# Kernel tuning notes

Hardware: AMD Instinct MI355X
Metric: run time of the kernel (lower is better)

## Reference

```python
import jax, jax.numpy as jnp
import numpy as np

PI = 3.141592653589793


def conv2d(x, w, b=None, padding=0, groups=1):
    out = jax.lax.conv_general_dilated(
        x, w, window_strides=(1, 1), padding=((padding, padding), (padding, padding)),
        dimension_numbers=('NCHW', 'OIHW', 'NCHW'), feature_group_count=groups)
    if b is not None:
        out = out + b.reshape(1, -1, 1, 1)
    return out


def group_norm(x, weight, bias, num_groups, eps=1e-5):
    B, C, H, W = x.shape
    xg = x.reshape(B, num_groups, C // num_groups, H, W)
    mean = xg.mean(axis=(2, 3, 4), keepdims=True)
    var = xg.var(axis=(2, 3, 4), keepdims=True)
    xg = (xg - mean) / jnp.sqrt(var + eps)
    return xg.reshape(B, C, H, W) * weight.reshape(1, -1, 1, 1) + bias.reshape(1, -1, 1, 1)


def l2norm(x, eps=1e-12):
    n = jnp.sqrt(jnp.sum(x * x, axis=1, keepdims=True))
    return x / jnp.maximum(n, eps)


def dense_sift(x):
    # kornia DenseSIFTDescriptor defaults: 8 angle bins, 4x4 spatial bins, bin size 4,
    # stride 1, padding 1, rootsift=True, clipval=0.2. Input (B,1,H,W) -> (B,128,H,W).
    eps = 1e-10
    B, C, H, W = x.shape
    # spatial_gradient(x, 'diff'), normalized: central differences / 2, replicate pad
    p = jnp.pad(x, ((0, 0), (0, 0), (1, 1), (1, 1)), mode='edge')
    gx = (p[:, :, 1:-1, 2:] - p[:, :, 1:-1, :-2]) * 0.5
    gy = (p[:, :, 2:, 1:-1] - p[:, :, :-2, 1:-1]) * 0.5
    mag = jnp.sqrt(gx * gx + gy * gy + eps)
    ori = jnp.arctan2(gy, gx + eps) + 2.0 * PI
    o_big = 8.0 * ori / (2.0 * PI)
    bo0f = jnp.floor(o_big)
    wo1 = o_big - bo0f
    bo0 = bo0f % 8
    bo1 = (bo0 + 1) % 8
    wo0m = (1.0 - wo1) * mag
    wo1m = wo1 * mag
    bins = jnp.arange(8, dtype=x.dtype).reshape(1, 8, 1, 1)
    # soft orientation-histogram binning -> (B,8,H,W)
    ang = jnp.where(bo0 == bins, wo0m, 0.0) + jnp.where(bo1 == bins, wo1m, 0.0)
    # triangular bin pooling kernel (ksize=4), depthwise conv, pad 2 -> (B,8,H+1,W+1)
    ks2 = 2.0
    xc2 = ks2 - jnp.abs(jnp.arange(4, dtype=x.dtype) + 0.5 - ks2)
    pk = jnp.outer(xc2, xc2) / (ks2 ** 2)
    pk = jnp.tile(pk.reshape(1, 1, 4, 4), (8, 1, 1, 1))
    pooled = jax.lax.conv_general_dilated(
        ang, pk, (1, 1), ((2, 2), (2, 2)),
        dimension_numbers=('NCHW', 'OIHW', 'NCHW'), feature_group_count=8)
    # PoolingConv with identity reshape kernel (k=4, pad=1) == 4x4 patch extraction
    pp = jnp.pad(pooled, ((0, 0), (0, 0), (1, 1), (1, 1)))
    patches = jnp.stack([pp[:, :, y:y + H, xx:xx + W]
                         for y in range(4) for xx in range(4)], axis=2)  # (B,8,16,H,W)
    out = patches.reshape(B, 128, H, W)
    out = jnp.clip(l2norm(out), 0.0, 0.2)
    out = l2norm(out)
    # rootsift: sqrt(L1-normalized + eps)
    l1 = jnp.sum(jnp.abs(out), axis=1, keepdims=True)
    out = jnp.sqrt(out / jnp.maximum(l1, 1e-12) + eps)
    return out


def gauss1d(ks, sigma):
    t = jnp.arange(ks, dtype=jnp.float32) - (ks - 1) / 2.0
    g = jnp.exp(-(t * t) / (2.0 * sigma * sigma))
    return g / g.sum()


def joint_bilateral_blur(inp, guidance, ks=5, sigma_color=0.1, sigma_space=(1.5, 1.5)):
    # kornia joint_bilateral_blur: border_type='reflect', color_distance_type='l1'
    B, C, H, W = inp.shape
    pad = ks // 2
    pi_ = jnp.pad(inp, ((0, 0), (0, 0), (pad, pad), (pad, pad)), mode='reflect')
    pg = jnp.pad(guidance, ((0, 0), (0, 0), (pad, pad), (pad, pad)), mode='reflect')

    def unfold(p):  # (B,C,H,W,ks*ks), flatten order (dy, dx)
        return jnp.stack([p[:, :, y:y + H, x:x + W]
                          for y in range(ks) for x in range(ks)], axis=-1)

    ui = unfold(pi_)
    ug = unfold(pg)
    diff = ug - guidance[..., None]
    cdist_sq = jnp.square(jnp.sum(jnp.abs(diff), axis=1, keepdims=True))  # L1 over channels, squared
    color_k = jnp.exp(-0.5 / (sigma_color ** 2) * cdist_sq)               # (B,1,H,W,K2)
    space_k = jnp.outer(gauss1d(ks, sigma_space[0]), gauss1d(ks, sigma_space[1])).reshape(1, 1, 1, 1, -1)
    kernel = space_k * color_k
    return (ui * kernel).sum(-1) / kernel.sum(-1)


def setup_inputs() -> dict:
    key = jax.random.key(0)
    ks = jax.random.split(key, 8)
    B, H, W = 4, 270, 512

    def wgt(k, shape, scale=0.05):
        return jax.random.normal(k, shape, dtype=jnp.float32) * scale

    z = lambda n: jnp.zeros((n,), dtype=jnp.float32)
    o = lambda n: jnp.ones((n,), dtype=jnp.float32)
    return {
        'x': jax.random.normal(ks[0], (B, 1, H, W), dtype=jnp.float32),
        'w1': wgt(ks[1], (64, 128, 5, 5)), 'b1': z(64), 'g1w': o(64), 'g1b': z(64),
        'w2': wgt(ks[2], (32, 64, 3, 3)), 'b2': z(32), 'g2w': o(32), 'g2b': z(32),
        'w3': wgt(ks[3], (16, 32, 3, 3)), 'b3': z(16), 'g3w': o(16), 'g3b': z(16),
        'w4': wgt(ks[4], (8, 16, 3, 3)), 'b4': z(8), 'g4w': o(8), 'g4b': z(8),
        'w5': wgt(ks[5], (2, 8, 3, 3)), 'b5': z(2),
        'sw1': wgt(ks[6], (32, 128, 1, 1)), 'sb1': z(32),
        'sw2': wgt(ks[7], (8, 32, 1, 1)), 'sb2': z(8),
    }


def reference(x, w1, b1, g1w, g1b, w2, b2, g2w, g2b, w3, b3, g3w, g3b,
              w4, b4, g4w, g4b, w5, b5, sw1, sb1, sw2, sb2):
    orig = x
    s = dense_sift(x)                                     # (B,128,H,W)
    h = jax.nn.relu(group_norm(conv2d(s, w1, b1, 2), g1w, g1b, 8))
    h = jax.nn.relu(group_norm(conv2d(h, w2, b2, 1), g2w, g2b, 8))
    h = h + conv2d(s, sw1, sb1, 0)                        # skip 1
    blk = h
    h = jax.nn.relu(group_norm(conv2d(h, w3, b3, 1), g3w, g3b, 4))
    h = jax.nn.relu(group_norm(conv2d(h, w4, b4, 1), g4w, g4b, 4))
    h = h + conv2d(blk, sw2, sb2, 0)                      # skip 2
    h = conv2d(h, w5, b5, 1)                              # (B,2,H,W)
    guide = jnp.tile(orig, (1, 2, 1, 1))
    h = joint_bilateral_blur(h, guide, ks=5, sigma_color=0.1, sigma_space=(1.5, 1.5))
    h = jnp.tanh(h)
    scale = jnp.array([0.436, 0.615], dtype=h.dtype).reshape(1, 2, 1, 1)
    return h * scale
```

## Files before the change

kernel.cpp:

```cpp
#include <hip/hip_runtime.h>

#define DEV __device__ __forceinline__

typedef __bf16 bf16x8 __attribute__((ext_vector_type(8)));
typedef float f32x4 __attribute__((ext_vector_type(4)));

union U8 { uint4 q; unsigned short u[8]; };

constexpr int BN = 4, H = 270, W = 512, HW = H * W;
constexpr int IH5 = 274, P5 = 516;
constexpr int IH3 = 272, P3 = 514;

DEV unsigned short f2bf(float f) {
  unsigned int u = __builtin_bit_cast(unsigned int, f);
  u = (u + 0x7FFFu + ((u >> 16) & 1u)) >> 16;
  return (unsigned short)u;
}
DEV float bf2f(unsigned short h) {
  return __builtin_bit_cast(float, (unsigned int)h << 16);
}

#define GLL16(g, l)                                                                        \
  __builtin_amdgcn_global_load_lds((const __attribute__((address_space(1))) void*)(g),     \
                                   (__attribute__((address_space(3))) void*)(l), 16, 0, 0)

DEV int swz(int row) { return ((row >> 1) & 3) << 4; }

__global__ void k_fill(float* __restrict__ out, int n, float v) {
  int i = blockIdx.x * 256 + threadIdx.x;
  if (i < n) out[i] = v;
}

template <int C, int PD>
__global__ void k_halo(unsigned short* __restrict__ buf, int IHt, int pitch, int nb_) {
  int vPerRow = pitch * C / 8;
  int topBot = 2 * PD * vPerRow;
  int sideV = PD * C / 8;
  int midRows = IHt - 2 * PD;
  int perS = topBot + midRows * 2 * sideV;
  int v = blockIdx.x * 256 + threadIdx.x;
  if (v >= nb_ * perS) return;
  int s = v / perS, r = v % perS;
  size_t base = (size_t)s * IHt * pitch * C;
  size_t off;
  if (r < topBot) {
    int half = r / (PD * vPerRow);
    int rr = r % (PD * vPerRow);
    off = ((size_t)(half ? (IHt - PD) : 0) * pitch * C) + (size_t)rr * 8;
  } else {
    int r2 = r - topBot;
    int row = r2 / (2 * sideV), c2 = r2 % (2 * sideV);
    int side = c2 / sideV, cc = c2 % sideV;
    off = ((size_t)(PD + row) * pitch + (side ? (pitch - PD) : 0)) * C + (size_t)cc * 8;
  }
  *(uint4*)(buf + base + off) = uint4{0, 0, 0, 0};
}

__global__ void k_sift_ang(const float* __restrict__ x, float* __restrict__ ang, int nTot) {
  int p = blockIdx.x * 256 + threadIdx.x;
  if (p >= nTot) return;
  int b = p / HW, r = p % HW, y = r / W, xx = r % W;
  const float* xb = x + (size_t)b * HW;
  float xm = xb[y * W + (xx > 0 ? xx - 1 : 0)];
  float xp = xb[y * W + (xx < W - 1 ? xx + 1 : W - 1)];
  float ym = xb[(y > 0 ? y - 1 : 0) * W + xx];
  float yp = xb[(y < H - 1 ? y + 1 : H - 1) * W + xx];
  float gx = (xp - xm) * 0.5f, gy = (yp - ym) * 0.5f;
  float mag = sqrtf(gx * gx + gy * gy + 1e-10f);
  float ori = atan2f(gy, gx + 1e-10f) + 6.2831855f;
  float o = (8.0f * ori) / 6.2831855f;
  float bo0f = floorf(o);
  float wo1 = o - bo0f;
  int b0 = ((int)bo0f) & 7;
  int b1 = (b0 + 1) & 7;
  float w0m = (1.0f - wo1) * mag, w1m = wo1 * mag;
  float v[8];
#pragma unroll
  for (int k = 0; k < 8; ++k)
    v[k] = (k == b0 ? w0m : 0.0f) + (k == b1 ? w1m : 0.0f);
  float4* o4 = (float4*)(ang + (size_t)p * 8);
  o4[0] = make_float4(v[0], v[1], v[2], v[3]);
  o4[1] = make_float4(v[4], v[5], v[6], v[7]);
}

__global__ void k_sift_pool(const float* __restrict__ ang, float* __restrict__ pooled, int nTot) {
  constexpr int PH = H + 1, PW = W + 1;
  int p = blockIdx.x * 256 + threadIdx.x;
  if (p >= nTot) return;
  int b = p / (PH * PW), r = p % (PH * PW), y = r / PW, xx = r % PW;
  float4 a0 = {0, 0, 0, 0}, a1 = {0, 0, 0, 0};
  const float xc2[4] = {0.5f, 1.5f, 1.5f, 0.5f};
#pragma unroll
  for (int ky = 0; ky < 4; ++ky) {
    int yy = y - 2 + ky;
    if (yy < 0 || yy >= H) continue;
#pragma unroll
    for (int kx = 0; kx < 4; ++kx) {
      int xs = xx - 2 + kx;
      if (xs < 0 || xs >= W) continue;
      float w = xc2[ky] * xc2[kx] * 0.25f;
      const float4* s4 = (const float4*)(ang + ((size_t)(b * H + yy) * W + xs) * 8);
      float4 v0 = s4[0], v1 = s4[1];
      a0.x += w * v0.x; a0.y += w * v0.y; a0.z += w * v0.z; a0.w += w * v0.w;
      a1.x += w * v1.x; a1.y += w * v1.y; a1.z += w * v1.z; a1.w += w * v1.w;
    }
  }
  float4* o4 = (float4*)(pooled + (size_t)p * 8);
  o4[0] = a0; o4[1] = a1;
}

__global__ void k_sift_desc(const float* __restrict__ pooled, unsigned short* __restrict__ spad) {
  constexpr int PH = H + 1, PW = W + 1;
  int tid = threadIdx.x;
  int wv = tid >> 6, lane = tid & 63;
  int p = blockIdx.x * 4 + wv;
  int b = p / HW, r = p % HW, yy = r / W, xx = r % W;
  int a = lane >> 3, jj = lane & 7;
  int j0 = jj * 2;
  int dy = j0 >> 2, dx = j0 & 3;
  int rr = yy + dy - 1;
  int c0 = xx + dx - 1, c1 = c0 + 1;
  bool rv = (rr >= 0 && rr <= H);
  int rc = min(max(rr, 0), H);
  const float* pb = pooled + ((size_t)(b * PH + rc) * PW) * 8 + a;
  float v0 = 0.0f, v1 = 0.0f;
  if (rv && c0 >= 0 && c0 <= W) v0 = pb[(size_t)c0 * 8];
  if (rv && c1 >= 0 && c1 <= W) v1 = pb[(size_t)c1 * 8];

  float n2 = v0 * v0 + v1 * v1;
#pragma unroll
  for (int m = 1; m < 64; m <<= 1) n2 += __shfl_xor(n2, m);
  float inv = 1.0f / fmaxf(sqrtf(n2), 1e-12f);
  v0 = fminf(v0 * inv, 0.2f);
  v1 = fminf(v1 * inv, 0.2f);
  float n2b = v0 * v0 + v1 * v1;
#pragma unroll
  for (int m = 1; m < 64; m <<= 1) n2b += __shfl_xor(n2b, m);
  inv = 1.0f / fmaxf(sqrtf(n2b), 1e-12f);
  v0 *= inv; v1 *= inv;
  float l1 = v0 + v1;
#pragma unroll
  for (int m = 1; m < 64; m <<= 1) l1 += __shfl_xor(l1, m);
  float il1 = 1.0f / fmaxf(l1, 1e-12f);
  v0 = sqrtf(v0 * il1 + 1e-10f);
  v1 = sqrtf(v1 * il1 + 1e-10f);
  unsigned int pk = (unsigned int)f2bf(v0) | ((unsigned int)f2bf(v1) << 16);
  *(unsigned int*)(spad + ((size_t)(b * IH5 + yy + 2) * P5 + xx + 2) * 128 + lane * 2) = pk;
}

template <int CIN, int COUT, int KS>
__global__ void k_prep(const float* __restrict__ w, unsigned short* __restrict__ wbuf) {
  int i = blockIdx.x * 256 + threadIdx.x;
  if (i >= KS * KS * COUT * CIN) return;
  int t = i / (COUT * CIN), r2 = i % (COUT * CIN), co = r2 / CIN, e = r2 % CIN;
  wbuf[i] = f2bf(w[(co * CIN + e) * (KS * KS) + t]);
}

template <int CIN, int COUT, int KS, int NG, int PADOFF, int MINB, bool FSKIP>
__launch_bounds__(512, MINB)
__global__ void k_convr(const unsigned short* __restrict__ in, int IHt, int ipitch,
                        const unsigned short* __restrict__ wtap,
                        const float* __restrict__ bias,
                        const unsigned short* __restrict__ wsk,
                        const float* __restrict__ skb,
                        unsigned short* __restrict__ outraw,
                        unsigned short* __restrict__ skraw,
                        float* __restrict__ part, int nbid) {
  constexpr int SLABPX = 512 + KS - 1;
  constexpr int KQ = CIN / 32;
  constexpr int NF = COUT / 16;
  constexpr int SLAB = SLABPX * 64;
  constexpr int SWQ = COUT * 64;
  constexpr int SWROW = KS * SWQ;
  constexpr int SSK = FSKIP ? 32 * 64 : 16;
  __shared__ __align__(16) unsigned char slabB[2][SLAB];
  __shared__ __align__(16) unsigned char wrowB[2][SWROW];
  __shared__ __align__(16) unsigned char wskB[2][SSK];
  __shared__ float red[8][16];

  int tid = threadIdx.x;
  int lane = tid & 63, wid = tid >> 6;
  int l15 = lane & 15, hi = lane >> 4;

  int bid = blockIdx.x;
  int q8 = nbid >> 3, r8 = nbid & 7;
  int xcd = bid & 7;
  int by = (xcd < r8 ? xcd * (q8 + 1) : r8 * (q8 + 1) + (xcd - r8) * q8) + (bid >> 3);
  int y = by % H, b = by / H;

  f32x4 acc[4][NF] = {};
  f32x4 ask[4][2] = {};

  auto stage = [&](int it, int pbuf) {
    int q = it / KS, ky = it % KS;
    const char* src = (const char*)(in + ((size_t)(b * IHt + y + ky + PADOFF) * ipitch + PADOFF) * CIN + q * 32);
    for (int d = tid * 16; d < SLAB; d += 8192) {
      int px = d >> 6, qb = d & 63;
      GLL16(src + px * (CIN * 2) + (qb ^ swz(px)), slabB[pbuf] + d);
    }
    const char* wsrc = (const char*)wtap + (size_t)(ky * KS) * (COUT * CIN * 2) + q * 64;
    for (int d = tid * 16; d < SWROW; d += 8192) {
      int kx = d / SWQ, rem = d % SWQ;
      int co = rem >> 6, qb = rem & 63;
      GLL16(wsrc + (size_t)kx * (COUT * CIN * 2) + co * (CIN * 2) + (qb ^ swz(co)), wrowB[pbuf] + d);
    }
  };
  auto stage_wsk = [&](int q, int pbuf) {
    const char* src = (const char*)wsk + q * 64;
    for (int d = tid * 16; d < 32 * 64; d += 8192) {
      int co = d >> 6, qb = d & 63;
      GLL16(src + co * (CIN * 2) + (qb ^ swz(co)), wskB[pbuf] + d);
    }
  };

  stage(0, 0);
  if constexpr (FSKIP) stage_wsk(0, 0);
  __syncthreads();

#pragma unroll 1
  for (int it = 0; it < KQ * KS; ++it) {
    int cur = it & 1;
    int q = it / KS, ky = it % KS;
    if (it + 1 < KQ * KS) {
      stage(it + 1, cur ^ 1);
      if (FSKIP && (it + 1) % KS == 0) stage_wsk((it + 1) / KS, ((it + 1) / KS) & 1);
    }
    const unsigned char* sl = slabB[cur];
    const unsigned char* wr = wrowB[cur];
    int koff = hi * 16;
#pragma unroll
    for (int kx = 0; kx < KS; ++kx) {
      bf16x8 af[4];
#pragma unroll
      for (int mi = 0; mi < 4; ++mi) {
        int px = wid * 64 + mi * 16 + l15 + kx;
        af[mi] = *(const bf16x8*)(sl + px * 64 + (koff ^ swz(px)));
      }
#pragma unroll
      for (int ni = 0; ni < NF; ++ni) {
        int co = ni * 16 + l15;
        bf16x8 bq = *(const bf16x8*)(wr + kx * SWQ + co * 64 + (koff ^ swz(co)));
#pragma unroll
        for (int mi = 0; mi < 4; ++mi)
          acc[mi][ni] = __builtin_amdgcn_mfma_f32_16x16x32_bf16(af[mi], bq, acc[mi][ni], 0, 0, 0);
      }
      if constexpr (FSKIP) {
        if (ky == KS / 2 && kx == KS / 2) {
#pragma unroll
          for (int ni = 0; ni < 2; ++ni) {
            int co = ni * 16 + l15;
            bf16x8 bq = *(const bf16x8*)(wskB[q & 1] + co * 64 + (koff ^ swz(co)));
#pragma unroll
            for (int mi = 0; mi < 4; ++mi)
              ask[mi][ni] = __builtin_amdgcn_mfma_f32_16x16x32_bf16(af[mi], bq, ask[mi][ni], 0, 0, 0);
          }
        }
      }
    }
    __syncthreads();
  }

#pragma unroll
  for (int ni = 0; ni < NF; ++ni) {
    float bv = bias[ni * 16 + l15];
#pragma unroll
    for (int mi = 0; mi < 4; ++mi)
#pragma unroll
      for (int rr = 0; rr < 4; ++rr)
        acc[mi][ni][rr] += bv;
  }
  unsigned short* op = outraw + ((size_t)(b * H + y) * W) * COUT;
#pragma unroll
  for (int mi = 0; mi < 4; ++mi)
#pragma unroll
    for (int rr = 0; rr < 4; ++rr) {
      int px = wid * 64 + mi * 16 + hi * 4 + rr;
#pragma unroll
      for (int ni = 0; ni < NF; ++ni)
        op[(size_t)px * COUT + ni * 16 + l15] = f2bf(acc[mi][ni][rr]);
    }
  if constexpr (FSKIP) {
    unsigned short* ops = skraw + ((size_t)(b * H + y) * W) * 32;
#pragma unroll
    for (int ni = 0; ni < 2; ++ni) {
      float bv = skb[ni * 16 + l15];
#pragma unroll
      for (int mi = 0; mi < 4; ++mi)
#pragma unroll
        for (int rr = 0; rr < 4; ++rr)
          ask[mi][ni][rr] += bv;
    }
#pragma unroll
    for (int mi = 0; mi < 4; ++mi)
#pragma unroll
      for (int rr = 0; rr < 4; ++rr) {
        int px = wid * 64 + mi * 16 + hi * 4 + rr;
#pragma unroll
        for (int ni = 0; ni < 2; ++ni)
          ops[(size_t)px * 32 + ni * 16 + l15] = f2bf(ask[mi][ni][rr]);
      }
  }
  if constexpr (NG > 0) {
    constexpr int GPC = COUT / NG;
#pragma unroll
    for (int ni = 0; ni < NF; ++ni) {
      float s = 0.0f, q2 = 0.0f;
#pragma unroll
      for (int mi = 0; mi < 4; ++mi)
#pragma unroll
        for (int rr = 0; rr < 4; ++rr) {
          float v = acc[mi][ni][rr];
          s += v; q2 += v * v;
        }
      s += __shfl_xor(s, 16); q2 += __shfl_xor(q2, 16);
      s += __shfl_xor(s, 32); q2 += __shfl_xor(q2, 32);
#pragma unroll
      for (int m = 1; m < GPC; m <<= 1) { s += __shfl_xor(s, m); q2 += __shfl_xor(q2, m); }
      if (hi == 0 && (l15 % GPC) == 0) {
        int g = ni * (16 / GPC) + l15 / GPC;
        red[wid][g] = s;
        red[wid][NG + g] = q2;
      }
    }
    __syncthreads();
    if (tid < 2 * NG) {
      float t = 0.0f;
#pragma unroll
      for (int wv2 = 0; wv2 < 8; ++wv2) t += red[wv2][tid];
      part[(size_t)by * (2 * NG) + tid] = t;
    }
  }
}

template <int COUT, int NG>
__global__ void k_gn_fin(const float* __restrict__ part, int NB,
                         const float* __restrict__ gw, const float* __restrict__ gb,
                         float* __restrict__ scale, float* __restrict__ shift, float invN) {
  constexpr int GPC = COUT / NG;
  int b = blockIdx.x / NG, g = blockIdx.x % NG;
  int lane = threadIdx.x;
  float s = 0.0f, q = 0.0f;
  for (int i = lane; i < NB; i += 64) {
    const float* pp = part + (size_t)(b * NB + i) * (2 * NG);
    s += pp[g]; q += pp[NG + g];
  }
#pragma unroll
  for (int m = 1; m < 64; m <<= 1) { s += __shfl_xor(s, m); q += __shfl_xor(q, m); }
  if (lane == 0) {
    float mean = s * invN;
    float var = q * invN - mean * mean;
    float rstd = rsqrtf(var + 1e-5f);
#pragma unroll
    for (int j = 0; j < GPC; ++j) {
      int c = g * GPC + j;
      float sc = gw[c] * rstd;
      scale[b * COUT + c] = sc;
      shift[b * COUT + c] = gb[c] - mean * sc;
    }
  }
}

template <int C, bool ADDSKIP>
__global__ void k_norm(const unsigned short* __restrict__ raw,
                       const unsigned short* __restrict__ skip,
                       const float* __restrict__ scale, const float* __restrict__ shift,
                       unsigned short* __restrict__ outpad) {
  int e = blockIdx.x * 256 + threadIdx.x;
  int idx = e * 8;
  int p = idx / C, c0 = idx % C;
  int b = p / HW, r = p % HW, y = r / W, xx = r % W;
  U8 v; v.q = *(const uint4*)(raw + (size_t)p * C + c0);
  U8 sk;
  if (ADDSKIP) sk.q = *(const uint4*)(skip + (size_t)p * C + c0);
  const float* sc = scale + b * C + c0;
  const float* sh = shift + b * C + c0;
  U8 o;
#pragma unroll
  for (int j = 0; j < 8; ++j) {
    float f = fmaxf(bf2f(v.u[j]) * sc[j] + sh[j], 0.0f);
    if (ADDSKIP) f += bf2f(sk.u[j]);
    o.u[j] = f2bf(f);
  }
  *(uint4*)(outpad + ((size_t)(b * IH3 + y + 1) * P3 + xx + 1) * C + c0) = o.q;
}

__global__ void k_conv4(const unsigned short* __restrict__ h3pad, const float* __restrict__ w4,
                        const float* __restrict__ b4, unsigned short* __restrict__ h4raw,
                        float* __restrict__ part) {
  __shared__ float wl[1152];
  __shared__ float red[4][8];
  for (int i = threadIdx.x; i < 1152; i += 256) {
    int t = i / 128, r2 = i % 128, ci = r2 >> 3, co = r2 & 7;
    wl[i] = w4[(co * 16 + ci) * 9 + t];
  }
  __syncthreads();
  int p = blockIdx.x * 256 + threadIdx.x;
  int b = p / HW, r = p % HW, y = r / W, xx = r % W;
  float acc[8];
#pragma unroll
  for (int co = 0; co < 8; ++co) acc[co] = b4[co];
#pragma unroll
  for (int t = 0; t < 9; ++t) {
    int ky = t / 3, kx = t % 3;
    const unsigned short* ip = h3pad + ((size_t)(b * IH3 + y + ky) * P3 + (xx + kx)) * 16;
    U8 u0, u1;
    u0.q = *(const uint4*)ip;
    u1.q = *(const uint4*)(ip + 8);
#pragma unroll
    for (int ci = 0; ci < 16; ++ci) {
      float iv = bf2f(ci < 8 ? u0.u[ci] : u1.u[ci - 8]);
#pragma unroll
      for (int co = 0; co < 8; ++co)
        acc[co] += iv * wl[t * 128 + ci * 8 + co];
    }
  }
  int lane = threadIdx.x & 63, wv = threadIdx.x >> 6;
  float s[4], q[4];
#pragma unroll
  for (int g = 0; g < 4; ++g) {
    s[g] = acc[2 * g] + acc[2 * g + 1];
    q[g] = acc[2 * g] * acc[2 * g] + acc[2 * g + 1] * acc[2 * g + 1];
  }
#pragma unroll
  for (int m = 1; m < 64; m <<= 1) {
#pragma unroll
    for (int g = 0; g < 4; ++g) { s[g] += __shfl_xor(s[g], m); q[g] += __shfl_xor(q[g], m); }
  }
  if (lane == 0) {
#pragma unroll
    for (int g = 0; g < 4; ++g) { red[wv][g] = s[g]; red[wv][4 + g] = q[g]; }
  }
  __syncthreads();
  if (threadIdx.x < 8)
    part[(size_t)blockIdx.x * 8 + threadIdx.x] =
        red[0][threadIdx.x] + red[1][threadIdx.x] + red[2][threadIdx.x] + red[3][threadIdx.x];
  U8 o;
#pragma unroll
  for (int co = 0; co < 8; ++co) o.u[co] = f2bf(acc[co]);
  *(uint4*)(h4raw + (size_t)p * 8) = o.q;
}

__global__ void k_norm4(const unsigned short* __restrict__ h4raw, const unsigned short* __restrict__ blkpad,
                        const float* __restrict__ scale, const float* __restrict__ shift,
                        const float* __restrict__ sw2, const float* __restrict__ sb2,
                        unsigned short* __restrict__ blk2pad) {
  __shared__ float wl[256];
  {
    int i = threadIdx.x;
    int ci = i >> 3, co = i & 7;
    wl[i] = sw2[co * 32 + ci];
  }
  __syncthreads();
  int p = blockIdx.x * 256 + threadIdx.x;
  int b = p / HW, r = p % HW, y = r / W, xx = r % W;
  float acc[8];
#pragma unroll
  for (int co = 0; co < 8; ++co) acc[co] = sb2[co];
  size_t cbase = ((size_t)(b * IH3 + y + 1) * P3 + (xx + 1));
  const unsigned short* bp = blkpad + cbase * 32;
#pragma unroll
  for (int half = 0; half < 4; ++half) {
    U8 u; u.q = *(const uint4*)(bp + half * 8);
#pragma unroll
    for (int j = 0; j < 8; ++j) {
      float iv = bf2f(u.u[j]);
      int ci = half * 8 + j;
#pragma unroll
      for (int co = 0; co < 8; ++co) acc[co] += iv * wl[ci * 8 + co];
    }
  }
  U8 hv; hv.q = *(const uint4*)(h4raw + (size_t)p * 8);
  U8 o;
#pragma unroll
  for (int co = 0; co < 8; ++co) {
    float f = fmaxf(bf2f(hv.u[co]) * scale[b * 8 + co] + shift[b * 8 + co], 0.0f) + acc[co];
    o.u[co] = f2bf(f);
  }
  *(uint4*)(blk2pad + cbase * 8) = o.q;
}

__global__ void k_conv5(const unsigned short* __restrict__ blk2pad, const float* __restrict__ w5,
                        const float* __restrict__ b5, float* __restrict__ h5) {
  __shared__ float wl[144];
  if (threadIdx.x < 144) {
    int i = threadIdx.x;
    int t = i / 16, r2 = i % 16, ci = r2 >> 1, co = r2 & 1;
    wl[i] = w5[(co * 8 + ci) * 9 + t];
  }
  __syncthreads();
  int p = blockIdx.x * 256 + threadIdx.x;
  int b = p / HW, r = p % HW, y = r / W, xx = r % W;
  float a0 = b5[0], a1 = b5[1];
#pragma unroll
  for (int t = 0; t < 9; ++t) {
    int ky = t / 3, kx = t % 3;
    const unsigned short* ip = blk2pad + ((size_t)(b * IH3 + y + ky) * P3 + (xx + kx)) * 8;
    U8 u; u.q = *(const uint4*)ip;
#pragma unroll
    for (int ci = 0; ci < 8; ++ci) {
      float iv = bf2f(u.u[ci]);
      a0 += iv * wl[t * 16 + ci * 2];
      a1 += iv * wl[t * 16 + ci * 2 + 1];
    }
  }
  h5[(size_t)p * 2] = a0;
  h5[(size_t)p * 2 + 1] = a1;
}

__global__ void k_bilateral(const float* __restrict__ h5, const float* __restrict__ x,
                            float* __restrict__ out, int nTot) {
  int p = blockIdx.x * 256 + threadIdx.x;
  if (p >= nTot) return;
  int b = p / HW, r = p % HW, y = r / W, xx = r % W;
  const float* xb = x + (size_t)b * HW;
  float xc = xb[r];
  float e1 = expf(-1.0f / 4.5f), e0 = expf(-4.0f / 4.5f);
  float gs = 1.0f + 2.0f * e1 + 2.0f * e0;
  float g[5] = {e0 / gs, e1 / gs, 1.0f / gs, e1 / gs, e0 / gs};
  float n0 = 0.0f, n1 = 0.0f, den = 0.0f;
#pragma unroll
  for (int dy = 0; dy < 5; ++dy) {
    int yn = y + dy - 2;
    yn = yn < 0 ? -yn : (yn >= H ? 2 * H - 2 - yn : yn);
#pragma unroll
    for (int dx = 0; dx < 5; ++dx) {
      int xn = xx + dx - 2;
      xn = xn < 0 ? -xn : (xn >= W ? 2 * W - 2 - xn : xn);
      float xv = xb[yn * W + xn];
      float d = xv - xc;
      float wgt = g[dy] * g[dx] * expf(-200.0f * d * d);
      den += wgt;
      const float* hp = h5 + ((size_t)(b * HW) + yn * W + xn) * 2;
      n0 += wgt * hp[0];
      n1 += wgt * hp[1];
    }
  }
  float o0 = tanhf(n0 / den) * 0.436f;
  float o1 = tanhf(n1 / den) * 0.615f;
  out[(size_t)(b * 2) * HW + r] = o0;
  out[(size_t)(b * 2 + 1) * HW + r] = o1;
}

extern "C" void kernel_launch(void* const* d_in, const int* in_sizes, int n_in,
                              void* d_out, int out_size, void* d_ws, size_t ws_size,
                              hipStream_t stream) {
  (void)in_sizes; (void)n_in; (void)out_size;
  const float* x   = (const float*)d_in[0];
  const float* w1  = (const float*)d_in[1];
  const float* b1  = (const float*)d_in[2];
  const float* g1w = (const float*)d_in[3];
  const float* g1b = (const float*)d_in[4];
  const float* w2  = (const float*)d_in[5];
  const float* b2  = (const float*)d_in[6];
  const float* g2w = (const float*)d_in[7];
  const float* g2b = (const float*)d_in[8];
  const float* w3  = (const float*)d_in[9];
  const float* b3  = (const float*)d_in[10];
  const float* g3w = (const float*)d_in[11];
  const float* g3b = (const float*)d_in[12];
  const float* w4  = (const float*)d_in[13];
  const float* b4  = (const float*)d_in[14];
  const float* g4w = (const float*)d_in[15];
  const float* g4b = (const float*)d_in[16];
  const float* w5  = (const float*)d_in[17];
  const float* b5  = (const float*)d_in[18];
  const float* sw1 = (const float*)d_in[19];
  const float* sb1 = (const float*)d_in[20];
  const float* sw2 = (const float*)d_in[21];
  const float* sb2 = (const float*)d_in[22];
  float* out = (float*)d_out;
  char* ws = (char*)d_ws;

  auto AL = [](size_t v) { return (v + 255) & ~(size_t)255; };
  const size_t sSPAD  = (size_t)IH5 * P5 * 128 * 2;
  const size_t sANG   = (size_t)HW * 8 * 4;
  const size_t sH1RAW = (size_t)HW * 64 * 2;
  const size_t sH1PAD = (size_t)IH3 * P3 * 64 * 2;
  const size_t sH2RAW = (size_t)HW * 32 * 2;
  const size_t sBLKP  = (size_t)IH3 * P3 * 32 * 2;
  const size_t sH3RAW = (size_t)HW * 16 * 2;
  const size_t sH3PAD = (size_t)IH3 * P3 * 16 * 2;
  const size_t sH4RAW = (size_t)HW * 8 * 2;
  const size_t sBLK2  = (size_t)IH3 * P3 * 8 * 2;

  int nb = 0;
  size_t offB = 0, offH1PAD = 0, offSmall = 0;
  const size_t smallFixed = AL(1024 * 1024) + AL((size_t)4 * 1080 * 16 * 4) + 8 * 4096;
  for (int cand = 4; cand >= 1; cand >>= 1) {
    size_t oB   = AL((size_t)cand * sSPAD);
    size_t oH1P = AL(oB + (size_t)cand * sH1RAW);
    size_t oS   = AL(oH1P + (size_t)cand * sH1PAD);
    size_t need = oS + smallFixed + AL((size_t)cand * sH2RAW);
    if (ws_size >= need) { nb = cand; offB = oB; offH1PAD = oH1P; offSmall = oS; break; }
  }
  if (nb == 0) {
    k_fill<<<(BN * 2 * HW + 255) / 256, 256, 0, stream>>>(out, BN * 2 * HW, 123.0f);
    return;
  }

  size_t oWB1  = offSmall;
  size_t oWB2  = AL(oWB1 + 25 * 64 * 128 * 2);
  size_t oWB3  = AL(oWB2 + 9 * 32 * 64 * 2);
  size_t oWBS  = AL(oWB3 + 9 * 16 * 32 * 2);
  size_t oPART = AL(oWBS + 32 * 128 * 2);
  size_t oSC1  = AL(oPART + (size_t)4 * 1080 * 16 * 4);
  size_t oSC2  = oSC1 + 4096, oSC3 = oSC2 + 4096, oSC4 = oSC3 + 4096;
  size_t oSK1  = oSC4 + 4096;

  unsigned short* wb1  = (unsigned short*)(ws + oWB1);
  unsigned short* wb2  = (unsigned short*)(ws + oWB2);
  unsigned short* wb3  = (unsigned short*)(ws + oWB3);
  unsigned short* wbs1 = (unsigned short*)(ws + oWBS);
  float* part = (float*)(ws + oPART);
  float* sc1 = (float*)(ws + oSC1); float* sh1 = sc1 + nb * 64;
  float* sc2 = (float*)(ws + oSC2); float* sh2 = sc2 + nb * 32;
  float* sc3 = (float*)(ws + oSC3); float* sh3 = sc3 + nb * 16;
  float* sc4 = (float*)(ws + oSC4); float* sh4 = sc4 + nb * 8;
  unsigned short* sk1 = (unsigned short*)(ws + oSK1);

  k_prep<128, 64, 5><<<800, 256, 0, stream>>>(w1, wb1);
  k_prep<64, 32, 3><<<72, 256, 0, stream>>>(w2, wb2);
  k_prep<32, 16, 3><<<18, 256, 0, stream>>>(w3, wb3);
  k_prep<128, 32, 1><<<16, 256, 0, stream>>>(sw1, wbs1);

  size_t t0 = AL((size_t)nb * sBLKP);
  size_t t1 = AL(t0 + (size_t)nb * sH3RAW);
  size_t t2 = AL(t1 + (size_t)nb * sH3PAD);
  size_t t3 = AL(t2 + (size_t)nb * sH4RAW);
  size_t t4 = AL(t3 + (size_t)nb * sBLK2);

  for (int b0 = 0; b0 < BN; b0 += nb) {
    const float* x_c = x + (size_t)b0 * HW;
    float* out_c = out + (size_t)b0 * 2 * HW;
    unsigned short* spad   = (unsigned short*)(ws);
    float*          ang    = (float*)(ws + offB);
    float*          pooled = (float*)(ws + AL(offB + (size_t)nb * sANG));
    unsigned short* h1raw  = (unsigned short*)(ws + offB);
    unsigned short* h1pad  = (unsigned short*)(ws + offH1PAD);
    unsigned short* h2raw  = (unsigned short*)(ws + offB);
    unsigned short* blkpad = (unsigned short*)(ws);
    unsigned short* h3raw  = (unsigned short*)(ws + t0);
    unsigned short* h3pad  = (unsigned short*)(ws + t1);
    unsigned short* h4raw  = (unsigned short*)(ws + t2);
    unsigned short* blk2   = (unsigned short*)(ws + t3);
    float*          h5     = (float*)(ws + t4);
    int nHW = nb * HW;
    int nbid = nb * H;

    k_halo<128, 2><<<(nb * 50304 + 255) / 256, 256, 0, stream>>>(spad, IH5, P5, nb);
    k_halo<64, 1><<<(nb * 12544 + 255) / 256, 256, 0, stream>>>(h1pad, IH3, P3, nb);

    k_sift_ang<<<nb * 540, 256, 0, stream>>>(x_c, ang, nHW);
    int nPP = nb * (H + 1) * (W + 1);
    k_sift_pool<<<(nPP + 255) / 256, 256, 0, stream>>>(ang, pooled, nPP);
    k_sift_desc<<<nHW / 4, 256, 0, stream>>>(pooled, spad);

    k_convr<128, 64, 5, 8, 0, 2, true><<<nbid, 512, 0, stream>>>(
        spad, IH5, P5, wb1, b1, wbs1, sb1, h1raw, sk1, part, nbid);
    k_gn_fin<64, 8><<<nb * 8, 64, 0, stream>>>(part, H, g1w, g1b, sc1, sh1, 1.0f / (8.0f * HW));
    k_norm<64, false><<<nb * 4320, 256, 0, stream>>>(h1raw, nullptr, sc1, sh1, h1pad);

    k_convr<64, 32, 3, 8, 0, 4, false><<<nbid, 512, 0, stream>>>(
        h1pad, IH3, P3, wb2, b2, nullptr, nullptr, h2raw, nullptr, part, nbid);
    k_gn_fin<32, 8><<<nb * 8, 64, 0, stream>>>(part, H, g2w, g2b, sc2, sh2, 1.0f / (4.0f * HW));

    k_halo<32, 1><<<(nb * 6272 + 255) / 256, 256, 0, stream>>>(blkpad, IH3, P3, nb);
    k_halo<16, 1><<<(nb * 3136 + 255) / 256, 256, 0, stream>>>(h3pad, IH3, P3, nb);
    k_halo<8, 1><<<(nb * 1568 + 255) / 256, 256, 0, stream>>>(blk2, IH3, P3, nb);

    k_norm<32, true><<<nb * 2160, 256, 0, stream>>>(h2raw, sk1, sc2, sh2, blkpad);

    k_convr<32, 16, 3, 4, 0, 4, false><<<nbid, 512, 0, stream>>>(
        blkpad, IH3, P3, wb3, b3, nullptr, nullptr, h3raw, nullptr, part, nbid);
    k_gn_fin<16, 4><<<nb * 4, 64, 0, stream>>>(part, H, g3w, g3b, sc3, sh3, 1.0f / (4.0f * HW));
    k_norm<16, false><<<nb * 1080, 256, 0, stream>>>(h3raw, nullptr, sc3, sh3, h3pad);

    k_conv4<<<nb * 540, 256, 0, stream>>>(h3pad, w4, b4, h4raw, part);
    k_gn_fin<8, 4><<<nb * 4, 64, 0, stream>>>(part, 540, g4w, g4b, sc4, sh4, 1.0f / (2.0f * HW));
    k_norm4<<<nb * 540, 256, 0, stream>>>(h4raw, blkpad, sc4, sh4, sw2, sb2, blk2);

    k_conv5<<<nb * 540, 256, 0, stream>>>(blk2, w5, b5, h5);
    k_bilateral<<<nb * 540, 256, 0, stream>>>(h5, x_c, out_c, nHW);
  }
}
```

Baseline: 729.0 us.

## Split conv1 into half-row blocks, fuse GN3 into conv4, simplify RootSIFT norm

Three separate changes. The first conv is now launched with 256-thread blocks, each covering half a row, which doubles the grid and shrinks the LDS slab so more blocks can run per CU. The GN3 normalise-plus-ReLU pass and its halo fill are folded into conv4, which reads the raw tensor and applies scale, shift and ReLU with bounds checks, saving one full write and read of the intermediate. The second L2 normalisation in the SIFT descriptor is dropped, since the L1 normalisation that follows cancels its scaling; this removes one cross-lane reduction per pixel, with only small floating-point differences.

```diff
diff --git a/kernel.cpp b/kernel.cpp
--- a/kernel.cpp
+++ b/kernel.cpp
@@ -133,17 +133,12 @@
   float inv = 1.0f / fmaxf(sqrtf(n2), 1e-12f);
   v0 = fminf(v0 * inv, 0.2f);
   v1 = fminf(v1 * inv, 0.2f);
-  float n2b = v0 * v0 + v1 * v1;
-#pragma unroll
-  for (int m = 1; m < 64; m <<= 1) n2b += __shfl_xor(n2b, m);
-  inv = 1.0f / fmaxf(sqrtf(n2b), 1e-12f);
-  v0 *= inv; v1 *= inv;
-  float l1 = v0 + v1;
-#pragma unroll
-  for (int m = 1; m < 64; m <<= 1) l1 += __shfl_xor(l1, m);
-  float il1 = 1.0f / fmaxf(l1, 1e-12f);
-  v0 = sqrtf(v0 * il1 + 1e-10f);
-  v1 = sqrtf(v1 * il1 + 1e-10f);
+  float S = v0 + v1;
+#pragma unroll
+  for (int m = 1; m < 64; m <<= 1) S += __shfl_xor(S, m);
+  float iS = 1.0f / fmaxf(S, 1e-12f);
+  v0 = sqrtf(v0 * iS + 1e-10f);
+  v1 = sqrtf(v1 * iS + 1e-10f);
   unsigned int pk = (unsigned int)f2bf(v0) | ((unsigned int)f2bf(v1) << 16);
   *(unsigned int*)(spad + ((size_t)(b * IH5 + yy + 2) * P5 + xx + 2) * 128 + lane * 2) = pk;
 }
@@ -156,8 +151,14 @@
   wbuf[i] = f2bf(w[(co * CIN + e) * (KS * KS) + t]);
 }
 
-template <int CIN, int COUT, int KS, int NG, int PADOFF, int MINB, bool FSKIP>
-__launch_bounds__(512, MINB)
+DEV int xcd_remap(int bid, int nbid) {
+  int q8 = nbid >> 3, r8 = nbid & 7;
+  int xcd = bid & 7;
+  return (xcd < r8 ? xcd * (q8 + 1) : r8 * (q8 + 1) + (xcd - r8) * q8) + (bid >> 3);
+}
+
+template <int CIN, int COUT, int KS, int NG, int MINW, bool FSKIP, int BMPX>
+__launch_bounds__(BMPX, MINW)
 __global__ void k_convr(const unsigned short* __restrict__ in, int IHt, int ipitch,
                         const unsigned short* __restrict__ wtap,
                         const float* __restrict__ bias,
@@ -166,40 +167,42 @@
                         unsigned short* __restrict__ outraw,
                         unsigned short* __restrict__ skraw,
                         float* __restrict__ part, int nbid) {
-  constexpr int SLABPX = 512 + KS - 1;
+  constexpr int NWV = BMPX / 64;
+  constexpr int NXB = 512 / BMPX;
+  constexpr int SLABPX = BMPX + KS - 1;
   constexpr int KQ = CIN / 32;
   constexpr int NF = COUT / 16;
   constexpr int SLAB = SLABPX * 64;
   constexpr int SWQ = COUT * 64;
   constexpr int SWROW = KS * SWQ;
   constexpr int SSK = FSKIP ? 32 * 64 : 16;
+  constexpr int STRIDE = BMPX * 16;
   __shared__ __align__(16) unsigned char slabB[2][SLAB];
   __shared__ __align__(16) unsigned char wrowB[2][SWROW];
   __shared__ __align__(16) unsigned char wskB[2][SSK];
-  __shared__ float red[8][16];
+  __shared__ float red[NWV][16];
 
   int tid = threadIdx.x;
   int lane = tid & 63, wid = tid >> 6;
   int l15 = lane & 15, hi = lane >> 4;
 
-  int bid = blockIdx.x;
-  int q8 = nbid >> 3, r8 = nbid & 7;
-  int xcd = bid & 7;
-  int by = (xcd < r8 ? xcd * (q8 + 1) : r8 * (q8 + 1) + (xcd - r8) * q8) + (bid >> 3);
-  int y = by % H, b = by / H;
+  int byl = xcd_remap(blockIdx.x, nbid);
+  int half = byl % NXB, rowid = byl / NXB;
+  int y = rowid % H, b = rowid / H;
+  int x0 = half * BMPX;
 
   f32x4 acc[4][NF] = {};
   f32x4 ask[4][2] = {};
 
   auto stage = [&](int it, int pbuf) {
     int q = it / KS, ky = it % KS;
-    const char* src = (const char*)(in + ((size_t)(b * IHt + y + ky + PADOFF) * ipitch + PADOFF) * CIN + q * 32);
-    for (int d = tid * 16; d < SLAB; d += 8192) {
+    const char* src = (const char*)(in + ((size_t)(b * IHt + y + ky) * ipitch + x0) * CIN + q * 32);
+    for (int d = tid * 16; d < SLAB; d += STRIDE) {
       int px = d >> 6, qb = d & 63;
       GLL16(src + px * (CIN * 2) + (qb ^ swz(px)), slabB[pbuf] + d);
     }
     const char* wsrc = (const char*)wtap + (size_t)(ky * KS) * (COUT * CIN * 2) + q * 64;
-    for (int d = tid * 16; d < SWROW; d += 8192) {
+    for (int d = tid * 16; d < SWROW; d += STRIDE) {
       int kx = d / SWQ, rem = d % SWQ;
       int co = rem >> 6, qb = rem & 63;
       GLL16(wsrc + (size_t)kx * (COUT * CIN * 2) + co * (CIN * 2) + (qb ^ swz(co)), wrowB[pbuf] + d);
@@ -207,7 +210,7 @@
   };
   auto stage_wsk = [&](int q, int pbuf) {
     const char* src = (const char*)wsk + q * 64;
-    for (int d = tid * 16; d < 32 * 64; d += 8192) {
+    for (int d = tid * 16; d < 32 * 64; d += STRIDE) {
       int co = d >> 6, qb = d & 63;
       GLL16(src + co * (CIN * 2) + (qb ^ swz(co)), wskB[pbuf] + d);
     }
@@ -269,7 +272,7 @@
       for (int rr = 0; rr < 4; ++rr)
         acc[mi][ni][rr] += bv;
   }
-  unsigned short* op = outraw + ((size_t)(b * H + y) * W) * COUT;
+  unsigned short* op = outraw + ((size_t)(b * H + y) * W + x0) * COUT;
 #pragma unroll
   for (int mi = 0; mi < 4; ++mi)
 #pragma unroll
@@ -280,7 +283,7 @@
         op[(size_t)px * COUT + ni * 16 + l15] = f2bf(acc[mi][ni][rr]);
     }
   if constexpr (FSKIP) {
-    unsigned short* ops = skraw + ((size_t)(b * H + y) * W) * 32;
+    unsigned short* ops = skraw + ((size_t)(b * H + y) * W + x0) * 32;
 #pragma unroll
     for (int ni = 0; ni < 2; ++ni) {
       float bv = skb[ni * 16 + l15];
@@ -326,8 +329,8 @@
     if (tid < 2 * NG) {
       float t = 0.0f;
 #pragma unroll
-      for (int wv2 = 0; wv2 < 8; ++wv2) t += red[wv2][tid];
-      part[(size_t)by * (2 * NG) + tid] = t;
+      for (int wv2 = 0; wv2 < NWV; ++wv2) t += red[wv2][tid];
+      part[(size_t)byl * (2 * NG) + tid] = t;
     }
   }
 }
@@ -384,15 +387,19 @@
   *(uint4*)(outpad + ((size_t)(b * IH3 + y + 1) * P3 + xx + 1) * C + c0) = o.q;
 }
 
-__global__ void k_conv4(const unsigned short* __restrict__ h3pad, const float* __restrict__ w4,
-                        const float* __restrict__ b4, unsigned short* __restrict__ h4raw,
-                        float* __restrict__ part) {
+__global__ void k_conv4(const unsigned short* __restrict__ h3raw, const float* __restrict__ w4,
+                        const float* __restrict__ b4,
+                        const float* __restrict__ sc3, const float* __restrict__ sh3,
+                        unsigned short* __restrict__ h4raw, float* __restrict__ part) {
   __shared__ float wl[1152];
+  __shared__ float scs[16], shs[16];
   __shared__ float red[4][8];
+  int b0 = (blockIdx.x * 256) / HW;
   for (int i = threadIdx.x; i < 1152; i += 256) {
     int t = i / 128, r2 = i % 128, ci = r2 >> 3, co = r2 & 7;
     wl[i] = w4[(co * 16 + ci) * 9 + t];
   }
+  if (threadIdx.x < 16) { scs[threadIdx.x] = sc3[b0 * 16 + threadIdx.x]; shs[threadIdx.x] = sh3[b0 * 16 + threadIdx.x]; }
   __syncthreads();
   int p = blockIdx.x * 256 + threadIdx.x;
   int b = p / HW, r = p % HW, y = r / W, xx = r % W;
@@ -402,13 +409,16 @@
 #pragma unroll
   for (int t = 0; t < 9; ++t) {
     int ky = t / 3, kx = t % 3;
-    const unsigned short* ip = h3pad + ((size_t)(b * IH3 + y + ky) * P3 + (xx + kx)) * 16;
+    int row = y + ky - 1, x = xx + kx - 1;
+    if (row < 0 || row >= H || x < 0 || x >= W) continue;
+    const unsigned short* ip = h3raw + ((size_t)(b * H + row) * W + x) * 16;
     U8 u0, u1;
     u0.q = *(const uint4*)ip;
     u1.q = *(const uint4*)(ip + 8);
 #pragma unroll
     for (int ci = 0; ci < 16; ++ci) {
-      float iv = bf2f(ci < 8 ? u0.u[ci] : u1.u[ci - 8]);
+      float raw = bf2f(ci < 8 ? u0.u[ci] : u1.u[ci - 8]);
+      float iv = fmaxf(raw * scs[ci] + shs[ci], 0.0f);
 #pragma unroll
       for (int co = 0; co < 8; ++co)
         acc[co] += iv * wl[t * 128 + ci * 8 + co];
@@ -640,12 +650,10 @@
     unsigned short* h2raw  = (unsigned short*)(ws + offB);
     unsigned short* blkpad = (unsigned short*)(ws);
     unsigned short* h3raw  = (unsigned short*)(ws + t0);
-    unsigned short* h3pad  = (unsigned short*)(ws + t1);
     unsigned short* h4raw  = (unsigned short*)(ws + t2);
     unsigned short* blk2   = (unsigned short*)(ws + t3);
     float*          h5     = (float*)(ws + t4);
     int nHW = nb * HW;
-    int nbid = nb * H;
 
     k_halo<128, 2><<<(nb * 50304 + 255) / 256, 256, 0, stream>>>(spad, IH5, P5, nb);
     k_halo<64, 1><<<(nb * 12544 + 255) / 256, 256, 0, stream>>>(h1pad, IH3, P3, nb);
@@ -655,28 +663,29 @@
     k_sift_pool<<<(nPP + 255) / 256, 256, 0, stream>>>(ang, pooled, nPP);
     k_sift_desc<<<nHW / 4, 256, 0, stream>>>(pooled, spad);
 
-    k_convr<128, 64, 5, 8, 0, 2, true><<<nbid, 512, 0, stream>>>(
-        spad, IH5, P5, wb1, b1, wbs1, sb1, h1raw, sk1, part, nbid);
-    k_gn_fin<64, 8><<<nb * 8, 64, 0, stream>>>(part, H, g1w, g1b, sc1, sh1, 1.0f / (8.0f * HW));
+    int n1 = nb * H * 2;
+    k_convr<128, 64, 5, 8, 2, true, 256><<<n1, 256, 0, stream>>>(
+        spad, IH5, P5, wb1, b1, wbs1, sb1, h1raw, sk1, part, n1);
+    k_gn_fin<64, 8><<<nb * 8, 64, 0, stream>>>(part, 2 * H, g1w, g1b, sc1, sh1, 1.0f / (8.0f * HW));
     k_norm<64, false><<<nb * 4320, 256, 0, stream>>>(h1raw, nullptr, sc1, sh1, h1pad);
 
-    k_convr<64, 32, 3, 8, 0, 4, false><<<nbid, 512, 0, stream>>>(
-        h1pad, IH3, P3, wb2, b2, nullptr, nullptr, h2raw, nullptr, part, nbid);
+    int n2 = nb * H;
+    k_convr<64, 32, 3, 8, 4, false, 512><<<n2, 512, 0, stream>>>(
+        h1pad, IH3, P3, wb2, b2, nullptr, nullptr, h2raw, nullptr, part, n2);
     k_gn_fin<32, 8><<<nb * 8, 64, 0, stream>>>(part, H, g2w, g2b, sc2, sh2, 1.0f / (4.0f * HW));
 
     k_halo<32, 1><<<(nb * 6272 + 255) / 256, 256, 0, stream>>>(blkpad, IH3, P3, nb);
-    k_halo<16, 1><<<(nb * 3136 + 255) / 256, 256, 0, stream>>>(h3pad, IH3, P3, nb);
     k_halo<8, 1><<<(nb * 1568 + 255) / 256, 256, 0, stream>>>(blk2, IH3, P3, nb);
 
     k_norm<32, true><<<nb * 2160, 256, 0, stream>>>(h2raw, sk1, sc2, sh2, blkpad);
 
-    k_convr<32, 16, 3, 4, 0, 4, false><<<nbid, 512, 0, stream>>>(
-        blkpad, IH3, P3, wb3, b3, nullptr, nullptr, h3raw, nullptr, part, nbid);
+    k_convr<32, 16, 3, 4, 4, false, 512><<<n2, 512, 0, stream>>>(
+        blkpad, IH3, P3, wb3, b3, nullptr, nullptr, h3raw, nullptr, part, n2);
     k_gn_fin<16, 4><<<nb * 4, 64, 0, stream>>>(part, H, g3w, g3b, sc3, sh3, 1.0f / (4.0f * HW));
-    k_norm<16, false><<<nb * 1080, 256, 0, stream>>>(h3raw, nullptr, sc3, sh3, h3pad);
-
-    k_conv4<<<nb * 540, 256, 0, stream>>>(h3pad, w4, b4, h4raw, part);
+
+    k_conv4<<<nb * 540, 256, 0, stream>>>(h3raw, w4, b4, sc3, sh3, h4raw, part);
     k_gn_fin<8, 4><<<nb * 4, 64, 0, stream>>>(part, 540, g4w, g4b, sc4, sh4, 1.0f / (2.0f * HW));
+
     k_norm4<<<nb * 540, 256, 0, stream>>>(h4raw, blkpad, sc4, sh4, sw2, sb2, blk2);
 
     k_conv5<<<nb * 540, 256, 0, stream>>>(blk2, w5, b5, h5);
```

Measured after the change: 664.0 us. 8.9% less time.
